# Optimization experiments

Measured on AMD Instinct MI355X. Metric: run time of the kernel, lower is better.

Reference implementation:

```python
import jax, jax.numpy as jnp
import numpy as np

B = 4096
IN = 1024   # complex input size (real tensor width = 2*IN)
H = 1024    # complex hidden size
G = 4       # gates: f, i, a, o


def _cproj(xr, xi, Wr, Wi, br, bi):
    # Complex linear over a stacked gate axis.
    # xr, xi: [B, D]; Wr, Wi: [G, H, D]; br, bi: [G, H] -> ([B,G,H], [B,G,H])
    zr = jnp.einsum('bd,god->bgo', xr, Wr) - jnp.einsum('bd,god->bgo', xi, Wi) + br
    zi = jnp.einsum('bd,god->bgo', xr, Wi) + jnp.einsum('bd,god->bgo', xi, Wr) + bi
    return zr, zi


def _ctimes(ar, ai, br, bi):
    # complex elementwise multiply (a_r + i a_i) * (b_r + i b_i)
    return ar * br - ai * bi, ar * bi + ai * br


def setup_inputs() -> dict:
    key = jax.random.key(0)
    ks = jax.random.split(key, 11)
    s_in = 1.0 / np.sqrt(2 * IN)
    s_h = 1.0 / np.sqrt(2 * H)
    return {
        'input': jax.random.normal(ks[0], (B, 2 * IN), jnp.float32),
        'h_x': jax.random.normal(ks[1], (B, 2 * H), jnp.float32),
        'c_x': jax.random.normal(ks[2], (B, 2 * H), jnp.float32),
        # input-side CLinear weights stacked over gates [f, i, a, o]
        'Uw_r': jax.random.normal(ks[3], (G, H, IN), jnp.float32) * s_in,
        'Uw_i': jax.random.normal(ks[4], (G, H, IN), jnp.float32) * s_in,
        'Ub_r': jax.random.normal(ks[5], (G, H), jnp.float32) * s_in,
        'Ub_i': jax.random.normal(ks[6], (G, H), jnp.float32) * s_in,
        # hidden-side CLinear weights stacked over gates [f, i, a, o]
        'Ww_r': jax.random.normal(ks[7], (G, H, H), jnp.float32) * s_h,
        'Ww_i': jax.random.normal(ks[8], (G, H, H), jnp.float32) * s_h,
        'Wb_r': jax.random.normal(ks[9], (G, H), jnp.float32) * s_h,
        'Wb_i': jax.random.normal(ks[10], (G, H), jnp.float32) * s_h,
    }


def reference(input, h_x, c_x, Uw_r, Uw_i, Ub_r, Ub_i, Ww_r, Ww_i, Wb_r, Wb_i):
    xr, xi = input[:, :IN], input[:, IN:]
    hr, hi = h_x[:, :H], h_x[:, H:]
    cr, ci = c_x[:, :H], c_x[:, H:]

    # fused gate projections: z = W(h) + U(x), complex-valued, [B, 4, H]
    zu_r, zu_i = _cproj(xr, xi, Uw_r, Uw_i, Ub_r, Ub_i)
    zh_r, zh_i = _cproj(hr, hi, Ww_r, Ww_i, Wb_r, Wb_i)
    zr = zu_r + zh_r
    zi = zu_i + zh_i

    # gate activations (applied elementwise to real and imag halves alike)
    fr, fi = jax.nn.sigmoid(zr[:, 0]), jax.nn.sigmoid(zi[:, 0])
    ir, ii = jax.nn.sigmoid(zr[:, 1]), jax.nn.sigmoid(zi[:, 1])
    ar, ai = jnp.tanh(zr[:, 2]), jnp.tanh(zi[:, 2])
    orr, oi = jax.nn.sigmoid(zr[:, 3]), jax.nn.sigmoid(zi[:, 3])

    cf_r, cf_i = _ctimes(cr, ci, fr, fi)
    ai_r, ai_i = _ctimes(ar, ai, ir, ii)
    ct_r, ct_i = cf_r + ai_r, cf_i + ai_i

    ht_r, ht_i = _ctimes(orr, oi, jnp.tanh(ct_r), jnp.tanh(ct_i))

    h_t = jnp.concatenate((ht_r, ht_i), axis=1)
    c_t = jnp.concatenate((ct_r, ct_i), axis=1)
    return h_t, c_t
```

## Files before the change

### kernel.cpp

```cpp
#include <hip/hip_runtime.h>
#include <cstddef>


typedef short bf16x8 __attribute__((ext_vector_type(8)));
typedef float f32x4  __attribute__((ext_vector_type(4)));
typedef unsigned int u32x4 __attribute__((ext_vector_type(4)));

static constexpr int KDIM = 4096;
static constexpr size_t HOFF = (size_t)4096 * 2048;

__device__ __forceinline__ unsigned short f2bf(float f) {
    unsigned u = __float_as_uint(f);
    u += 0x7FFF + ((u >> 16) & 1);
    return (unsigned short)(u >> 16);
}

__device__ __forceinline__ u32x4 pack8(float4 a, float4 b) {
    u32x4 v;
    v.x = (unsigned)f2bf(a.x) | ((unsigned)f2bf(a.y) << 16);
    v.y = (unsigned)f2bf(a.z) | ((unsigned)f2bf(a.w) << 16);
    v.z = (unsigned)f2bf(b.x) | ((unsigned)f2bf(b.y) << 16);
    v.w = (unsigned)f2bf(b.z) | ((unsigned)f2bf(b.w) << 16);
    return v;
}

__device__ __forceinline__ float4 neg4(float4 v) {
    return make_float4(-v.x, -v.y, -v.z, -v.w);
}

__device__ __forceinline__ void async16(const void* g, void* l) {
    __builtin_amdgcn_global_load_lds(
        (const __attribute__((address_space(1))) unsigned int*)g,
        (__attribute__((address_space(3))) unsigned int*)l,
        16, 0, 0);
}

__device__ __forceinline__ float sigm(float x) { return 1.0f / (1.0f + __expf(-x)); }
__device__ __forceinline__ float tanh_(float x) {
    float e = __expf(2.0f * x);
    return (e - 1.0f) / (e + 1.0f);
}

__global__ __launch_bounds__(256) void pack_all(
    const float* __restrict__ input, const float* __restrict__ hx,
    const float* __restrict__ Uw_r, const float* __restrict__ Uw_i,
    const float* __restrict__ Ww_r, const float* __restrict__ Ww_i,
    const float* __restrict__ Ub_r, const float* __restrict__ Ub_i,
    const float* __restrict__ Wb_r, const float* __restrict__ Wb_i,
    unsigned short* __restrict__ Xb, unsigned short* __restrict__ Wb16,
    float* __restrict__ biasp) {
    int bid = blockIdx.x;
    if (bid < 8192) {
        int idx = bid * 256 + threadIdx.x;
        int r    = idx >> 9;
        int gcol = (idx & 511) * 8;
        const float* src = (gcol < 2048) ? (input + (size_t)r * 2048 + gcol)
                                         : (hx    + (size_t)r * 2048 + (gcol - 2048));
        float4 f0 = *(const float4*)src;
        float4 f1 = *(const float4*)(src + 4);
        *(u32x4*)(Xb + (size_t)idx * 8) = pack8(f0, f1);
    } else {
        int idx = (bid - 8192) * 256 + threadIdx.x;
        int np = idx >> 9;
        int c8 = idx & 511;
        int k  = c8 * 8;
        int o = np >> 2, g = np & 3;
        int q = k >> 10, d = k & 1023;
        size_t sidx = (size_t)g * (1024 * 1024) + (size_t)o * 1024 + d;
        const float* srcR = (q < 2 ? Uw_r : Ww_r) + sidx;
        const float* srcI = (q < 2 ? Uw_i : Ww_i) + sidx;
        float4 r0 = *(const float4*)srcR; float4 r1 = *(const float4*)(srcR + 4);
        float4 i0 = *(const float4*)srcI; float4 i1 = *(const float4*)(srcI + 4);
        int n0 = o * 8 + g * 2;
        u32x4 p0, p1;
        if (q & 1) { p0 = pack8(neg4(i0), neg4(i1)); p1 = pack8(r0, r1); }
        else       { p0 = pack8(r0, r1);             p1 = pack8(i0, i1); }
        *(u32x4*)(Wb16 + (size_t)n0 * KDIM + k)       = p0;
        *(u32x4*)(Wb16 + (size_t)(n0 + 1) * KDIM + k) = p1;
        if (c8 == 0) {
            size_t bi = (size_t)g * 1024 + o;
            biasp[n0]     = Ub_r[bi] + Wb_r[bi];
            biasp[n0 + 1] = Ub_i[bi] + Wb_i[bi];
        }
    }
}

__global__ __launch_bounds__(512) void clstm_gemm(
    const unsigned short* __restrict__ Xb,
    const unsigned short* __restrict__ Wb,
    const float* __restrict__ biasp,
    const float* __restrict__ c_x,
    float* __restrict__ out) {
    extern __shared__ char smem[];

    const int tid  = threadIdx.x;
    const int lane = tid & 63;
    const int wave = tid >> 6;
    const int wm = wave >> 2, wn = wave & 3;
    const int quad = lane >> 4, col16 = lane & 15;

    const int bid = blockIdx.x;
    const int swz = (bid & 7) * 64 + (bid >> 3);
    const int st = swz >> 5, wi = swz & 31;
    const int mtile = (st & 3) * 4 + (wi & 3);
    const int ntile = (st >> 2) * 8 + (wi >> 2);

    const int srow  = tid >> 3;
    const int sslot = tid & 7;
    const unsigned short* pa[4];
    const unsigned short* pb[4];
#pragma unroll
    for (int i = 0; i < 4; ++i) {
        const int rowA = i * 64 + srow;
        const int c = sslot ^ (rowA & 7);
        pa[i] = Xb + (size_t)(mtile * 256 + rowA) * KDIM + c * 8;
        pb[i] = Wb + (size_t)(ntile * 256 + rowA) * KDIM + c * 8;
    }

    f32x4 acc[8][4] = {};

#pragma unroll
    for (int i = 0; i < 4; ++i) {
        async16(pa[i], smem + i * 8192 + wave * 1024);
        async16(pb[i], smem + 32768 + i * 8192 + wave * 1024);
        pa[i] += 64; pb[i] += 64;
    }

    const int rA0 = wm * 128 + col16;
    const int rB0 = wn * 64 + col16;

#pragma unroll 2
    for (int kt = 0; kt < 64; ++kt) {
        char* sA  = smem + (kt & 1) * 65536;
        char* sB  = sA + 32768;
        char* sAn = smem + (((kt & 1) ^ 1)) * 65536;
        char* sBn = sAn + 32768;

        if (kt < 63) {
#pragma unroll
            for (int i = 0; i < 4; ++i) {
                async16(pa[i], sAn + i * 8192 + wave * 1024);
                async16(pb[i], sBn + i * 8192 + wave * 1024);
                pa[i] += 64; pb[i] += 64;
            }
            asm volatile("s_waitcnt vmcnt(8)" ::: "memory");
        } else {
            asm volatile("s_waitcnt vmcnt(0)" ::: "memory");
        }
        __builtin_amdgcn_s_barrier();

        bf16x8 bfr[4][2];
#pragma unroll
        for (int n = 0; n < 4; ++n)
#pragma unroll
            for (int ks = 0; ks < 2; ++ks) {
                const int r = rB0 + n * 16;
                const int ch = (ks * 4 + quad) ^ (r & 7);
                bfr[n][ks] = *(const bf16x8*)(sB + r * 128 + ch * 16);
            }

#pragma unroll
        for (int p = 0; p < 4; ++p) {
            bf16x8 af[2][2];
#pragma unroll
            for (int f = 0; f < 2; ++f)
#pragma unroll
                for (int ks = 0; ks < 2; ++ks) {
                    const int r = rA0 + p * 32 + f * 16;
                    const int ch = (ks * 4 + quad) ^ (r & 7);
                    af[f][ks] = *(const bf16x8*)(sA + r * 128 + ch * 16);
                }
            __builtin_amdgcn_s_barrier();
            __builtin_amdgcn_s_setprio(1);
#pragma unroll
            for (int f = 0; f < 2; ++f)
#pragma unroll
                for (int n = 0; n < 4; ++n) {
                    acc[p * 2 + f][n] = __builtin_amdgcn_mfma_f32_16x16x32_bf16(
                        af[f][0], bfr[n][0], acc[p * 2 + f][n], 0, 0, 0);
                    acc[p * 2 + f][n] = __builtin_amdgcn_mfma_f32_16x16x32_bf16(
                        af[f][1], bfr[n][1], acc[p * 2 + f][n], 0, 0, 0);
                }
            __builtin_amdgcn_s_setprio(0);
            __builtin_amdgcn_s_barrier();
        }
    }

    __syncthreads();
    float* zs = (float*)(smem + wave * 8192);
    const float* bp = biasp + ntile * 256 + wn * 64;
    const int o_idx = lane & 3;
    const int rgrp  = lane >> 2;

#pragma unroll
    for (int pass = 0; pass < 8; ++pass) {
        const int seg = pass >> 1;
        const int h   = pass & 1;
#pragma unroll
        for (int mf2 = 0; mf2 < 2; ++mf2)
#pragma unroll
            for (int tl = 0; tl < 2; ++tl) {
                int nf = h * 2 + tl;
                int colz = tl * 16 + col16;
#pragma unroll
                for (int r = 0; r < 4; ++r)
                    zs[(mf2 * 16 + quad * 4 + r) * 40 + colz] = acc[seg * 2 + mf2][nf][r];
            }

        float4 bb0 = *(const float4*)(bp + h * 32 + o_idx * 8);
        float4 bb1 = *(const float4*)(bp + h * 32 + o_idx * 8 + 4);
        int o_glob = ntile * 32 + wn * 8 + h * 4 + o_idx;

#pragma unroll
        for (int t = 0; t < 2; ++t) {
            int rowz = rgrp + t * 16;
            const float* zp = zs + rowz * 40 + o_idx * 8;
            float4 z0 = *(const float4*)zp;
            float4 z1 = *(const float4*)(zp + 4);
            int b = mtile * 256 + wm * 128 + seg * 32 + rowz;

            float fr = sigm(z0.x + bb0.x), fi = sigm(z0.y + bb0.y);
            float ir = sigm(z0.z + bb0.z), ii = sigm(z0.w + bb0.w);
            float ar = tanh_(z1.x + bb1.x), ai = tanh_(z1.y + bb1.y);
            float og_r = sigm(z1.z + bb1.z), og_i = sigm(z1.w + bb1.w);

            float cr = c_x[(size_t)b * 2048 + o_glob];
            float ci = c_x[(size_t)b * 2048 + 1024 + o_glob];

            float ct_r = (cr * fr - ci * fi) + (ar * ir - ai * ii);
            float ct_i = (cr * fi + ci * fr) + (ar * ii + ai * ir);
            float tr = tanh_(ct_r), ti = tanh_(ct_i);
            float ht_r = og_r * tr - og_i * ti;
            float ht_i = og_r * ti + og_i * tr;

            out[(size_t)b * 2048 + o_glob]               = ht_r;
            out[(size_t)b * 2048 + 1024 + o_glob]        = ht_i;
            out[HOFF + (size_t)b * 2048 + o_glob]        = ct_r;
            out[HOFF + (size_t)b * 2048 + 1024 + o_glob] = ct_i;
        }
        if (pass < 7)
            asm volatile("s_waitcnt lgkmcnt(0)" ::: "memory");
    }
}

extern "C" void kernel_launch(void* const* d_in, const int* in_sizes, int n_in,
                              void* d_out, int out_size, void* d_ws, size_t ws_size,
                              hipStream_t stream) {
    const float* input = (const float*)d_in[0];
    const float* h_x   = (const float*)d_in[1];
    const float* c_x   = (const float*)d_in[2];
    const float* Uw_r  = (const float*)d_in[3];
    const float* Uw_i  = (const float*)d_in[4];
    const float* Ub_r  = (const float*)d_in[5];
    const float* Ub_i  = (const float*)d_in[6];
    const float* Ww_r  = (const float*)d_in[7];
    const float* Ww_i  = (const float*)d_in[8];
    const float* Wb_r  = (const float*)d_in[9];
    const float* Wb_i  = (const float*)d_in[10];
    float* out = (float*)d_out;

    unsigned short* Xb   = (unsigned short*)d_ws;
    unsigned short* Wb16 = Xb + (size_t)4096 * 4096;
    float* biasp = (float*)(Wb16 + (size_t)8192 * 4096);

    static bool s_attr = false;
    if (!s_attr) {
        hipFuncSetAttribute((const void*)clstm_gemm,
                            hipFuncAttributeMaxDynamicSharedMemorySize, 131072);
        s_attr = true;
    }

    pack_all<<<16384, 256, 0, stream>>>(input, h_x, Uw_r, Uw_i, Ww_r, Ww_i,
                                        Ub_r, Ub_i, Wb_r, Wb_i, Xb, Wb16, biasp);
    clstm_gemm<<<512, 512, 131072, stream>>>(Xb, Wb16, biasp, c_x, out);
}
```

Measured before the change: 457.5 us.

## Interleave async tile loads with MFMA and double-buffer A fragments in registers

```diff
diff --git a/kernel.cpp b/kernel.cpp
--- a/kernel.cpp
+++ b/kernel.cpp
@@ -136,17 +136,7 @@
         char* sAn = smem + (((kt & 1) ^ 1)) * 65536;
         char* sBn = sAn + 32768;
 
-        if (kt < 63) {
-#pragma unroll
-            for (int i = 0; i < 4; ++i) {
-                async16(pa[i], sAn + i * 8192 + wave * 1024);
-                async16(pb[i], sBn + i * 8192 + wave * 1024);
-                pa[i] += 64; pb[i] += 64;
-            }
-            asm volatile("s_waitcnt vmcnt(8)" ::: "memory");
-        } else {
-            asm volatile("s_waitcnt vmcnt(0)" ::: "memory");
-        }
+        asm volatile("s_waitcnt vmcnt(0)" ::: "memory");
         __builtin_amdgcn_s_barrier();
 
         bf16x8 bfr[4][2];
@@ -158,31 +148,45 @@
                 const int ch = (ks * 4 + quad) ^ (r & 7);
                 bfr[n][ks] = *(const bf16x8*)(sB + r * 128 + ch * 16);
             }
+        bf16x8 af[2][2][2];
+#pragma unroll
+        for (int f = 0; f < 2; ++f)
+#pragma unroll
+            for (int ks = 0; ks < 2; ++ks) {
+                const int r = rA0 + f * 16;
+                const int ch = (ks * 4 + quad) ^ (r & 7);
+                af[0][f][ks] = *(const bf16x8*)(sA + r * 128 + ch * 16);
+            }
 
 #pragma unroll
         for (int p = 0; p < 4; ++p) {
-            bf16x8 af[2][2];
-#pragma unroll
-            for (int f = 0; f < 2; ++f)
-#pragma unroll
-                for (int ks = 0; ks < 2; ++ks) {
-                    const int r = rA0 + p * 32 + f * 16;
-                    const int ch = (ks * 4 + quad) ^ (r & 7);
-                    af[f][ks] = *(const bf16x8*)(sA + r * 128 + ch * 16);
-                }
-            __builtin_amdgcn_s_barrier();
+            const int cur = p & 1, nxt = cur ^ 1;
+            if (p < 3) {
+#pragma unroll
+                for (int f = 0; f < 2; ++f)
+#pragma unroll
+                    for (int ks = 0; ks < 2; ++ks) {
+                        const int r = rA0 + (p + 1) * 32 + f * 16;
+                        const int ch = (ks * 4 + quad) ^ (r & 7);
+                        af[nxt][f][ks] = *(const bf16x8*)(sA + r * 128 + ch * 16);
+                    }
+            }
+            if (kt < 63) {
+                async16(pa[p], sAn + p * 8192 + wave * 1024);
+                async16(pb[p], sBn + p * 8192 + wave * 1024);
+                pa[p] += 64; pb[p] += 64;
+            }
             __builtin_amdgcn_s_setprio(1);
 #pragma unroll
             for (int f = 0; f < 2; ++f)
 #pragma unroll
                 for (int n = 0; n < 4; ++n) {
                     acc[p * 2 + f][n] = __builtin_amdgcn_mfma_f32_16x16x32_bf16(
-                        af[f][0], bfr[n][0], acc[p * 2 + f][n], 0, 0, 0);
+                        af[cur][f][0], bfr[n][0], acc[p * 2 + f][n], 0, 0, 0);
                     acc[p * 2 + f][n] = __builtin_amdgcn_mfma_f32_16x16x32_bf16(
-                        af[f][1], bfr[n][1], acc[p * 2 + f][n], 0, 0, 0);
+                        af[cur][f][1], bfr[n][1], acc[p * 2 + f][n], 0, 0, 0);
                 }
             __builtin_amdgcn_s_setprio(0);
-            __builtin_amdgcn_s_barrier();
         }
     }
 
```

New measurement: 433.0 us. 1.06x faster.
